# Kernel optimization log

Hardware: AMD Instinct MI355X
Metric: run time of the kernel (lower is better)

Reference implementation:

```python
import jax, jax.numpy as jnp
import numpy as np

N, E, IN, H = 10000, 320000, 128, 64

def setup_inputs() -> dict:
    key = jax.random.key(0)
    ks = jax.random.split(key, 6)
    x = jax.random.normal(ks[0], (N, IN), dtype=jnp.float32)
    edge_index = jax.random.randint(ks[1], (2, E), 0, N)
    edge_weight = jax.random.uniform(ks[2], (E,), dtype=jnp.float32)
    W_rel = jax.random.normal(ks[3], (IN, H), dtype=jnp.float32) / np.float32(np.sqrt(IN))
    W_root = jax.random.normal(ks[4], (IN, H), dtype=jnp.float32) / np.float32(np.sqrt(IN))
    b = jnp.zeros((H,), dtype=jnp.float32)
    return {"x": x, "edge_index": edge_index, "edge_weight": edge_weight,
            "W_rel": W_rel, "W_root": W_root, "b": b}

def reference(x, edge_index, edge_weight, W_rel, W_root, b):
    # GraphConv (PyG): out_i = W_rel @ sum_{j->i} e_ji * x_j + W_root @ x_i + b
    src, dst = edge_index[0], edge_index[1]
    msgs = x[src] * edge_weight[:, None]                    # [E, IN] gather
    agg = jax.ops.segment_sum(msgs, dst, num_segments=N)    # [N, IN] scatter-add
    z = agg @ W_rel + x @ W_root + b                        # [N, H]
    # (activation=None, dropout inactive in eval, no BN)
    adj = jax.nn.sigmoid(z @ z.T)                           # [N, N] inner-product decoder
    return adj, z
```

## Files before the change

kernel.cpp:

```cpp
#include <hip/hip_runtime.h>
#include <hip/hip_bf16.h>
#include <stdint.h>

#define N_NODES 10000
#define N_EDGES 320000
#define DIM_IN  128
#define DIM_H   64
#define SSTR    72
#define CSTR    132

typedef __attribute__((ext_vector_type(8))) short  short8;
typedef __attribute__((ext_vector_type(8))) unsigned short ushort8;
typedef __attribute__((ext_vector_type(4))) float  f32x4;

__device__ __forceinline__ unsigned short f2bf(float f) {
    union { float f; unsigned int i; } v; v.f = f;
    unsigned int u = v.i;
    return (unsigned short)((u + 0x7fffu + ((u >> 16) & 1u)) >> 16);
}

__global__ void hist_kernel(const int* __restrict__ ei, int* __restrict__ deg) {
    int e = blockIdx.x * blockDim.x + threadIdx.x;
    if (e < N_EDGES) atomicAdd(&deg[ei[N_EDGES + e]], 1);
}

__global__ void __launch_bounds__(1024) scan_kernel(const int* __restrict__ deg,
                                                    int* __restrict__ offs,
                                                    int* __restrict__ cursor) {
    __shared__ int part[1024];
    int t = threadIdx.x;
    int base = t * 10;
    int local[10];
    int s = 0;
    for (int i = 0; i < 10; ++i) {
        int idx = base + i;
        int d = (idx < N_NODES) ? deg[idx] : 0;
        local[i] = d; s += d;
    }
    part[t] = s;
    __syncthreads();
    for (int o = 1; o < 1024; o <<= 1) {
        int add = (t >= o) ? part[t - o] : 0;
        __syncthreads();
        part[t] += add;
        __syncthreads();
    }
    int run = part[t] - s;
    for (int i = 0; i < 10; ++i) {
        int idx = base + i;
        if (idx < N_NODES) { offs[idx] = run; cursor[idx] = run; run += local[i]; }
    }
    if (t == 1023) offs[N_NODES] = part[1023];
}

__global__ void bucket_kernel(const int* __restrict__ ei,
                              const float* __restrict__ ew,
                              int* __restrict__ cursor,
                              int2* __restrict__ swsrt) {
    int e = blockIdx.x * blockDim.x + threadIdx.x;
    if (e < N_EDGES) {
        int d = ei[N_EDGES + e];
        int slot = atomicAdd(&cursor[d], 1);
        int2 pay;
        pay.x = ei[e];
        pay.y = __float_as_int(ew[e]);
        swsrt[slot] = pay;
    }
}

__global__ void __launch_bounds__(64) agg_dense_kernel(
    const float* __restrict__ x,
    const int2* __restrict__ swsrt,
    const float* __restrict__ wrel,
    const float* __restrict__ wroot,
    const float* __restrict__ bias,
    const int* __restrict__ offs,
    float* __restrict__ out,
    unsigned short* __restrict__ zb)
{
    int i = blockIdx.x;
    int lane = threadIdx.x;
    int half = lane >> 5;
    int l32  = lane & 31;
    __shared__ float aggL[DIM_IN];
    __shared__ float xL[DIM_IN];

    int beg = offs[i], end = offs[i + 1];
    f32x4 a = (f32x4)0.f;
    #pragma unroll 4
    for (int p = beg + half; p < end; p += 2) {
        int2 sw = swsrt[p];
        float w = __int_as_float(sw.y);
        f32x4 xv = *(const f32x4*)(x + (size_t)sw.x * DIM_IN + l32 * 4);
        a += xv * w;
    }
    f32x4 b;
    b.x = __shfl_xor(a.x, 32);
    b.y = __shfl_xor(a.y, 32);
    b.z = __shfl_xor(a.z, 32);
    b.w = __shfl_xor(a.w, 32);
    a += b;
    if (half == 0) *(f32x4*)&aggL[l32 * 4] = a;

    float2 xi = ((const float2*)(x + (size_t)i * DIM_IN))[lane];
    xL[2 * lane]     = xi.x;
    xL[2 * lane + 1] = xi.y;
    __syncthreads();

    int h = lane;
    float acc = bias[h];
    for (int k = 0; k < DIM_IN; ++k) {
        acc += aggL[k] * wrel[k * DIM_H + h];
        acc += xL[k]   * wroot[k * DIM_H + h];
    }
    out[(size_t)N_NODES * N_NODES + (size_t)i * DIM_H + h] = acc;
    zb[(size_t)i * DIM_H + h] = f2bf(acc);
}

__global__ void __launch_bounds__(256) gemm_sig_kernel(
    const unsigned short* __restrict__ zb, float* __restrict__ out)
{
    __shared__ __align__(16) unsigned short sAB[2 * 128 * SSTR];
    unsigned short* sA = sAB;
    unsigned short* sB = sAB + 128 * SSTR;

    int t    = threadIdx.x;
    int lane = t & 63;
    int wave = t >> 6;
    int wm = wave >> 1, wn = wave & 1;
    int j0 = blockIdx.x * 128;
    int i0 = blockIdx.y * 128;
    int l15  = lane & 15;
    int quad = lane >> 4;

    #pragma unroll
    for (int pass = 0; pass < 4; ++pass) {
        int c   = pass * 256 + t;
        int row = c >> 3;
        int c8  = (c & 7) << 3;
        int ga = i0 + row; if (ga >= N_NODES) ga = N_NODES - 1;
        int gb = j0 + row; if (gb >= N_NODES) gb = N_NODES - 1;
        ushort8 va = *(const ushort8*)(zb + (size_t)ga * DIM_H + c8);
        ushort8 vb = *(const ushort8*)(zb + (size_t)gb * DIM_H + c8);
        *(ushort8*)(&sA[row * SSTR + c8]) = va;
        *(ushort8*)(&sB[row * SSTR + c8]) = vb;
    }
    __syncthreads();

    f32x4 acc[4][4];
    #pragma unroll
    for (int a = 0; a < 4; ++a)
        #pragma unroll
        for (int b = 0; b < 4; ++b) acc[a][b] = (f32x4)0.f;

    #pragma unroll
    for (int s = 0; s < 2; ++s) {
        int kb = quad * 8 + s * 32;
        short8 af[4], bfr[4];
        #pragma unroll
        for (int mi = 0; mi < 4; ++mi)
            af[mi] = *(const short8*)(&sA[(wm * 64 + mi * 16 + l15) * SSTR + kb]);
        #pragma unroll
        for (int ni = 0; ni < 4; ++ni)
            bfr[ni] = *(const short8*)(&sB[(wn * 64 + ni * 16 + l15) * SSTR + kb]);
        #pragma unroll
        for (int mi = 0; mi < 4; ++mi)
            #pragma unroll
            for (int ni = 0; ni < 4; ++ni)
                acc[mi][ni] = __builtin_amdgcn_mfma_f32_16x16x32_bf16(
                    af[mi], bfr[ni], acc[mi][ni], 0, 0, 0);
    }

    float* sC = (float*)sAB;
    #pragma unroll
    for (int half = 0; half < 2; ++half) {
        __syncthreads();
        if (wm == half) {
            #pragma unroll
            for (int mi = 0; mi < 4; ++mi)
                #pragma unroll
                for (int ni = 0; ni < 4; ++ni)
                    #pragma unroll
                    for (int r = 0; r < 4; ++r)
                        sC[(mi * 16 + quad * 4 + r) * CSTR + wn * 64 + ni * 16 + l15]
                            = acc[mi][ni][r];
        }
        __syncthreads();
        int i0h = i0 + half * 64;
        #pragma unroll
        for (int it = 0; it < 8; ++it) {
            int idx = it * 256 + t;
            int row = idx >> 5;
            int c4  = (idx & 31) << 2;
            f32x4 v = *(const f32x4*)&sC[row * CSTR + c4];
            f32x4 sg;
            sg.x = 1.0f / (1.0f + __expf(-v.x));
            sg.y = 1.0f / (1.0f + __expf(-v.y));
            sg.z = 1.0f / (1.0f + __expf(-v.z));
            sg.w = 1.0f / (1.0f + __expf(-v.w));
            int grow = i0h + row;
            int gcol = j0 + c4;
            if (grow < N_NODES && gcol + 3 < N_NODES) {
                __builtin_nontemporal_store(
                    sg, (f32x4*)(out + (size_t)grow * N_NODES + gcol));
            }
        }
    }
}

extern "C" void kernel_launch(void* const* d_in, const int* in_sizes, int n_in,
                              void* d_out, int out_size, void* d_ws, size_t ws_size,
                              hipStream_t stream) {
    const float* x     = (const float*)d_in[0];
    const int*   ei    = (const int*)d_in[1];
    const float* ew    = (const float*)d_in[2];
    const float* wrel  = (const float*)d_in[3];
    const float* wroot = (const float*)d_in[4];
    const float* bias  = (const float*)d_in[5];
    float* out = (float*)d_out;

    char* base = (char*)d_ws;
    unsigned short* zb = (unsigned short*)(base);
    int2* swsrt  = (int2*)(base + 1280000);
    int* deg     = (int*)(base + 3840000);
    int* offs    = (int*)(base + 3880000);
    int* cursor  = (int*)(base + 3920004);

    hipMemsetAsync(deg, 0, N_NODES * sizeof(int), stream);
    hist_kernel<<<(N_EDGES + 255) / 256, 256, 0, stream>>>(ei, deg);
    scan_kernel<<<1, 1024, 0, stream>>>(deg, offs, cursor);
    bucket_kernel<<<(N_EDGES + 255) / 256, 256, 0, stream>>>(ei, ew, cursor, swsrt);
    agg_dense_kernel<<<N_NODES, 64, 0, stream>>>(x, swsrt, wrel, wroot, bias,
                                                 offs, out, zb);
    dim3 grid((N_NODES + 127) / 128, (N_NODES + 127) / 128);
    gemm_sig_kernel<<<grid, 256, 0, stream>>>(zb, out);
}
```

Measured before the change: 504.2 us.

## Project features through W_rel before aggregation to halve gather width

```diff
diff --git a/kernel.cpp b/kernel.cpp
--- a/kernel.cpp
+++ b/kernel.cpp
@@ -68,53 +68,70 @@
     }
 }
 
-__global__ void __launch_bounds__(64) agg_dense_kernel(
+__global__ void __launch_bounds__(64) feat_kernel(
     const float* __restrict__ x,
-    const int2* __restrict__ swsrt,
     const float* __restrict__ wrel,
     const float* __restrict__ wroot,
     const float* __restrict__ bias,
+    float* __restrict__ xr,
+    float* __restrict__ xw)
+{
+    int i = blockIdx.x;
+    int lane = threadIdx.x;
+    __shared__ float xL[DIM_IN];
+    float2 xi = ((const float2*)(x + (size_t)i * DIM_IN))[lane];
+    xL[2 * lane]     = xi.x;
+    xL[2 * lane + 1] = xi.y;
+    __syncthreads();
+
+    float ar = 0.f, aw = bias[lane];
+    for (int k = 0; k < DIM_IN; ++k) {
+        float xv = xL[k];
+        ar += xv * wrel[k * DIM_H + lane];
+        aw += xv * wroot[k * DIM_H + lane];
+    }
+    xr[(size_t)i * DIM_H + lane] = ar;
+    xw[(size_t)i * DIM_H + lane] = aw;
+}
+
+__global__ void __launch_bounds__(64) agg_kernel(
+    const float* __restrict__ xr,
+    const float* __restrict__ xw,
+    const int2* __restrict__ swsrt,
     const int* __restrict__ offs,
     float* __restrict__ out,
     unsigned short* __restrict__ zb)
 {
     int i = blockIdx.x;
     int lane = threadIdx.x;
-    int half = lane >> 5;
-    int l32  = lane & 31;
-    __shared__ float aggL[DIM_IN];
-    __shared__ float xL[DIM_IN];
+    int q   = lane >> 4;
+    int l16 = lane & 15;
 
     int beg = offs[i], end = offs[i + 1];
     f32x4 a = (f32x4)0.f;
     #pragma unroll 4
-    for (int p = beg + half; p < end; p += 2) {
+    for (int p = beg + q; p < end; p += 4) {
         int2 sw = swsrt[p];
         float w = __int_as_float(sw.y);
-        f32x4 xv = *(const f32x4*)(x + (size_t)sw.x * DIM_IN + l32 * 4);
-        a += xv * w;
+        f32x4 v = *(const f32x4*)(xr + (size_t)sw.x * DIM_H + l16 * 4);
+        a += v * w;
     }
     f32x4 b;
-    b.x = __shfl_xor(a.x, 32);
-    b.y = __shfl_xor(a.y, 32);
-    b.z = __shfl_xor(a.z, 32);
-    b.w = __shfl_xor(a.w, 32);
+    b.x = __shfl_xor(a.x, 16); b.y = __shfl_xor(a.y, 16);
+    b.z = __shfl_xor(a.z, 16); b.w = __shfl_xor(a.w, 16);
     a += b;
-    if (half == 0) *(f32x4*)&aggL[l32 * 4] = a;
-
-    float2 xi = ((const float2*)(x + (size_t)i * DIM_IN))[lane];
-    xL[2 * lane]     = xi.x;
-    xL[2 * lane + 1] = xi.y;
-    __syncthreads();
-
-    int h = lane;
-    float acc = bias[h];
-    for (int k = 0; k < DIM_IN; ++k) {
-        acc += aggL[k] * wrel[k * DIM_H + h];
-        acc += xL[k]   * wroot[k * DIM_H + h];
-    }
-    out[(size_t)N_NODES * N_NODES + (size_t)i * DIM_H + h] = acc;
-    zb[(size_t)i * DIM_H + h] = f2bf(acc);
+    b.x = __shfl_xor(a.x, 32); b.y = __shfl_xor(a.y, 32);
+    b.z = __shfl_xor(a.z, 32); b.w = __shfl_xor(a.w, 32);
+    a += b;
+
+    if (q == 0) {
+        f32x4 w4 = *(const f32x4*)(xw + (size_t)i * DIM_H + l16 * 4);
+        f32x4 z4 = a + w4;
+        *(f32x4*)(out + (size_t)N_NODES * N_NODES + (size_t)i * DIM_H + l16 * 4) = z4;
+        ushort4 h;
+        h.x = f2bf(z4.x); h.y = f2bf(z4.y); h.z = f2bf(z4.z); h.w = f2bf(z4.w);
+        *(ushort4*)(zb + (size_t)i * DIM_H + l16 * 4) = h;
+    }
 }
 
 __global__ void __launch_bounds__(256) gemm_sig_kernel(
@@ -221,17 +238,19 @@
 
     char* base = (char*)d_ws;
     unsigned short* zb = (unsigned short*)(base);
-    int2* swsrt  = (int2*)(base + 1280000);
-    int* deg     = (int*)(base + 3840000);
-    int* offs    = (int*)(base + 3880000);
-    int* cursor  = (int*)(base + 3920004);
+    float* xr    = (float*)(base + 1280000);
+    float* xw    = (float*)(base + 3840000);
+    int2* swsrt  = (int2*)(base + 6400000);
+    int* deg     = (int*)(base + 8960000);
+    int* offs    = (int*)(base + 9000000);
+    int* cursor  = (int*)(base + 9040004);
 
     hipMemsetAsync(deg, 0, N_NODES * sizeof(int), stream);
     hist_kernel<<<(N_EDGES + 255) / 256, 256, 0, stream>>>(ei, deg);
     scan_kernel<<<1, 1024, 0, stream>>>(deg, offs, cursor);
     bucket_kernel<<<(N_EDGES + 255) / 256, 256, 0, stream>>>(ei, ew, cursor, swsrt);
-    agg_dense_kernel<<<N_NODES, 64, 0, stream>>>(x, swsrt, wrel, wroot, bias,
-                                                 offs, out, zb);
+    feat_kernel<<<N_NODES, 64, 0, stream>>>(x, wrel, wroot, bias, xr, xw);
+    agg_kernel<<<N_NODES, 64, 0, stream>>>(xr, xw, swsrt, offs, out, zb);
     dim3 grid((N_NODES + 127) / 128, (N_NODES + 127) / 128);
     gemm_sig_kernel<<<grid, 256, 0, stream>>>(zb, out);
 }
```

After: 499.6 us. No clear change (-0.9%).
